# Kernel optimization log

Hardware: AMD Instinct MI355X
Metric: run time of the kernel (lower is better)

The kernel has to match this reference:

```python
import jax, jax.numpy as jnp
import numpy as np

NUM_HEADS = 16
NUM_KV_HEADS = 4
HEAD_DIM = 128
ROPE_DIMS = 64
EPS = 1.1920929e-07  # torch.finfo(float32).eps, used by F.rms_norm(eps=None)


def rms_norm(x):
    ms = jnp.mean(jnp.square(x), axis=-1, keepdims=True)
    return x * jax.lax.rsqrt(ms + EPS)


def apply_rotary(x, cos, sin):
    # x: [..., s, rope_dims]; cos/sin: [s, rope_dims//2]
    h = x.shape[-1] // 2
    x1, x2 = x[..., :h], x[..., h:]
    return jnp.concatenate([x1 * cos + x2 * sin, -x1 * sin + x2 * cos], axis=-1)


def setup_inputs() -> dict:
    key = jax.random.key(0)
    ks = jax.random.split(key, 5)
    b, s, d = 2, 2048, 2048
    return {
        "x": jax.random.normal(ks[0], (b, s, d), jnp.float32),
        "q_w": jax.random.normal(ks[1], (d, d), jnp.float32) * 0.02,
        "k_w": jax.random.normal(ks[2], (NUM_KV_HEADS * HEAD_DIM, d), jnp.float32) * 0.02,
        "v_w": jax.random.normal(ks[3], (NUM_KV_HEADS * HEAD_DIM, d), jnp.float32) * 0.02,
        "out_w": jax.random.normal(ks[4], (d, d), jnp.float32) * 0.02,
        "q_gain": jnp.full((NUM_HEADS,), 12.0, jnp.float32),
    }


def reference(x, q_w, k_w, v_w, out_w, q_gain):
    b, s, d = x.shape
    g = NUM_HEADS // NUM_KV_HEADS

    q = (x @ q_w.T).reshape(b, s, NUM_HEADS, HEAD_DIM).transpose(0, 2, 1, 3)
    k = (x @ k_w.T).reshape(b, s, NUM_KV_HEADS, HEAD_DIM).transpose(0, 2, 1, 3)
    v = (x @ v_w.T).reshape(b, s, NUM_KV_HEADS, HEAD_DIM).transpose(0, 2, 1, 3)

    q = rms_norm(q)
    k = rms_norm(k)

    # partial rotary embedding
    t = jnp.arange(s, dtype=jnp.float32)
    inv_freq = 1.0 / (10000.0 ** (jnp.arange(0, ROPE_DIMS, 2, dtype=jnp.float32) / ROPE_DIMS))
    f = jnp.outer(t, inv_freq)                      # [s, rope_dims//2]
    cos, sin = jnp.cos(f), jnp.sin(f)

    q = jnp.concatenate([apply_rotary(q[..., :ROPE_DIMS], cos, sin), q[..., ROPE_DIMS:]], axis=-1)
    q = q * q_gain[None, :, None, None]
    k = jnp.concatenate([apply_rotary(k[..., :ROPE_DIMS], cos, sin), k[..., ROPE_DIMS:]], axis=-1)

    # GQA-native causal attention (no repeated K/V materialization)
    qg = q.reshape(b, NUM_KV_HEADS, g, s, HEAD_DIM)
    scale = 1.0 / jnp.sqrt(jnp.float32(HEAD_DIM))
    scores = jnp.einsum("bkgqd,bkld->bkgql", qg, k) * scale
    causal = jnp.tril(jnp.ones((s, s), bool))
    scores = jnp.where(causal, scores, jnp.finfo(scores.dtype).min)
    p = jax.nn.softmax(scores, axis=-1)
    y = jnp.einsum("bkgql,bkld->bkgqd", p, v)       # [b, kvh, g, s, hd]
    y = y.reshape(b, NUM_HEADS, s, HEAD_DIM).transpose(0, 2, 1, 3).reshape(b, s, d)
    return y @ out_w.T
```

## Files before the change

### kernel.cpp

```cpp
#include <hip/hip_runtime.h>
#include <cmath>


#define S_LEN 2048
#define DMODEL 2048
#define NH 16
#define NKV 4
#define HD 128

#define NEG_SENT -1.0e30f
#define QK_SCALE 0.08838834764831845f
#define RESCALE_THR 8.0f

typedef _Float16 f16x8 __attribute__((ext_vector_type(8)));
typedef float f32x4 __attribute__((ext_vector_type(4)));

static __device__ __forceinline__ short f2h(float f) {
  _Float16 h = (_Float16)f;
  return *(short*)&h;
}
static __device__ __forceinline__ float h2f(short s) {
  _Float16 h = *(_Float16*)&s;
  return (float)h;
}

static __device__ __forceinline__ void stage16(const short* g, short* ldsbase) {
  __builtin_amdgcn_global_load_lds(
      (const __attribute__((address_space(1))) void*)g,
      (__attribute__((address_space(3))) void*)ldsbase, 16, 0, 0);
}

__global__ __launch_bounds__(256) void f32_to_f16_all(
    const float* __restrict__ s0, const float* __restrict__ s1,
    const float* __restrict__ s2, const float* __restrict__ s3,
    const float* __restrict__ s4, short* __restrict__ d0,
    short* __restrict__ d1, short* __restrict__ d2, short* __restrict__ d3,
    short* __restrict__ d4) {
  int u = blockIdx.x * 256 + threadIdx.x;
  const float* src;
  short* dst;
  int off;
  if (u < 2097152) {
    src = s0; dst = d0; off = u;
  } else if (u < 3145728) {
    src = s1; dst = d1; off = u - 2097152;
  } else if (u < 3407872) {
    src = s2; dst = d2; off = u - 3145728;
  } else if (u < 3670016) {
    src = s3; dst = d3; off = u - 3407872;
  } else {
    src = s4; dst = d4; off = u - 3670016;
  }
  float4 v = *reinterpret_cast<const float4*>(src + (size_t)off * 4);
  short4 o;
  o.x = f2h(v.x); o.y = f2h(v.y); o.z = f2h(v.z); o.w = f2h(v.w);
  *reinterpret_cast<short4*>(dst + (size_t)off * 4) = o;
}

template <bool F32OUT>
static __device__ __forceinline__ void gemm_core(const short* __restrict__ A,
                                                 const short* __restrict__ W,
                                                 void* __restrict__ Cv,
                                                 int N, int K, int bm, int bn) {
  __shared__ __align__(16) short As[2][128][64];
  __shared__ __align__(16) short Ws[2][128][64];
  const int tid = threadIdx.x;
  const int wave = tid >> 6, lane = tid & 63;
  const int quad = lane >> 4, l16 = lane & 15;
  const int wm = (wave >> 1) * 64, wn = (wave & 1) * 64;

  f32x4 acc[4][4];
#pragma unroll
  for (int i = 0; i < 4; i++)
#pragma unroll
    for (int j = 0; j < 4; j++) acc[i][j] = f32x4{0.f, 0.f, 0.f, 0.f};

  const int srow = wave * 8 + (lane >> 3);
  const int scol = (lane & 7) * 8;

  const int NT = K >> 6;

  auto stage_tile = [&](int t, int s) {
    const int k0 = t * 64;
#pragma unroll
    for (int i = 0; i < 4; i++) {
      stage16(A + (size_t)(bm + srow + i * 32) * K + k0 + scol,
              &As[s][wave * 8 + i * 32][0]);
      stage16(W + (size_t)(bn + srow + i * 32) * K + k0 + scol,
              &Ws[s][wave * 8 + i * 32][0]);
    }
  };

  stage_tile(0, 0);

  for (int t = 0; t < NT; t++) {
    const int s = t & 1;
    if (t + 1 < NT) {
      stage_tile(t + 1, s ^ 1);
      asm volatile("s_waitcnt vmcnt(8)" ::: "memory");
    } else {
      asm volatile("s_waitcnt vmcnt(0)" ::: "memory");
    }
    __builtin_amdgcn_s_barrier();

#pragma unroll
    for (int kk = 0; kk < 64; kk += 32) {
      f16x8 af[4], bfr[4];
#pragma unroll
      for (int mi = 0; mi < 4; mi++)
        af[mi] = *reinterpret_cast<const f16x8*>(&As[s][wm + mi * 16 + l16][kk + quad * 8]);
#pragma unroll
      for (int ni = 0; ni < 4; ni++)
        bfr[ni] = *reinterpret_cast<const f16x8*>(&Ws[s][wn + ni * 16 + l16][kk + quad * 8]);
#pragma unroll
      for (int mi = 0; mi < 4; mi++)
#pragma unroll
        for (int ni = 0; ni < 4; ni++)
          acc[mi][ni] = __builtin_amdgcn_mfma_f32_16x16x32_f16(af[mi], bfr[ni], acc[mi][ni], 0, 0, 0);
    }

    if (t + 1 < NT) {
      asm volatile("s_waitcnt lgkmcnt(0)" ::: "memory");
      __builtin_amdgcn_sched_barrier(0);
      __builtin_amdgcn_s_barrier();
    }
  }

#pragma unroll
  for (int mi = 0; mi < 4; mi++)
#pragma unroll
    for (int ni = 0; ni < 4; ni++) {
      int gr = bm + wm + mi * 16 + quad * 4;
      int gc = bn + wn + ni * 16 + l16;
#pragma unroll
      for (int r = 0; r < 4; r++) {
        if (F32OUT)
          ((float*)Cv)[(size_t)(gr + r) * N + gc] = acc[mi][ni][r];
        else
          ((short*)Cv)[(size_t)(gr + r) * N + gc] = f2h(acc[mi][ni][r]);
      }
    }
}

template <bool F32OUT>
__global__ __launch_bounds__(256) void gemm_bt(const short* __restrict__ A,
                                               const short* __restrict__ W,
                                               void* __restrict__ Cv,
                                               int N, int K) {
  gemm_core<F32OUT>(A, W, Cv, N, K, blockIdx.x * 128, blockIdx.y * 128);
}

__global__ __launch_bounds__(256) void gemm_qkv(const short* __restrict__ A,
                                                const short* __restrict__ Wq,
                                                const short* __restrict__ Wk,
                                                const short* __restrict__ Wv,
                                                short* __restrict__ Cq,
                                                short* __restrict__ Ck,
                                                short* __restrict__ Cvp,
                                                int K) {
  const int y = blockIdx.y;
  const short* W;
  short* C;
  int N, bn;
  if (y < 16) {
    W = Wq; C = Cq; N = 2048; bn = y * 128;
  } else if (y < 20) {
    W = Wk; C = Ck; N = 512; bn = (y - 16) * 128;
  } else {
    W = Wv; C = Cvp; N = 512; bn = (y - 20) * 128;
  }
  gemm_core<false>(A, W, (void*)C, N, K, blockIdx.x * 128, bn);
}

__global__ __launch_bounds__(256) void postproc(const short* __restrict__ src,
                                                short* __restrict__ dst,
                                                const float* __restrict__ gain,
                                                int n_heads, int mode) {
  int gw = blockIdx.x * 4 + (threadIdx.x >> 6);
  int lane = threadIdx.x & 63;
  int head = gw % n_heads;
  int token = gw / n_heads;
  int s = token & (S_LEN - 1);
  int b = token >> 11;
  const short* sp = src + (size_t)token * (n_heads * HD) + head * HD;
  float v0 = h2f(sp[lane]);
  float v1 = h2f(sp[lane + 64]);
  float ss = v0 * v0 + v1 * v1;
#pragma unroll
  for (int off = 1; off < 64; off <<= 1) ss += __shfl_xor(ss, off, 64);
  float sc = rsqrtf(ss * (1.0f / 128.0f) + 1.1920929e-07f);
  v0 *= sc;
  v1 *= sc;
  int i = lane & 31;
  float inv = powf(10000.0f, -((float)(2 * i) * (1.0f / 64.0f)));
  float f = (float)s * inv;
  float cs, sn;
  sincosf(f, &sn, &cs);
  float partner = __shfl_xor(v0, 32, 64);
  v0 = (lane < 32) ? (v0 * cs + partner * sn) : (v0 * cs - partner * sn);
  if (mode == 2) {
    float g = gain[head] * QK_SCALE;
    v0 *= g;
    v1 *= g;
  }
  short* dp = dst + ((size_t)(b * n_heads + head) * S_LEN + s) * HD;
  dp[lane] = f2h(v0);
  dp[lane + 64] = f2h(v1);
}

__global__ __launch_bounds__(256) void v_transpose(const short* __restrict__ src,
                                                   short* __restrict__ dst) {
  __shared__ __align__(16) short t[64][72];
  const int tid = threadIdx.x;
  const int s0 = blockIdx.x * 64;
  const int d0 = blockIdx.y * 64;
#pragma unroll
  for (int i = 0; i < 2; i++) {
    int r = (tid >> 3) + i * 32;
    int c = (tid & 7) * 8;
    *reinterpret_cast<int4*>(&t[r][c]) =
        *reinterpret_cast<const int4*>(src + (size_t)(s0 + r) * 512 + d0 + c);
  }
  __syncthreads();
  const int b = s0 >> 11;
  const int sbase = s0 & (S_LEN - 1);
#pragma unroll
  for (int i = 0; i < 2; i++) {
    int dr = (tid >> 3) + i * 32;
    int sc8 = (tid & 7) * 8;
    int d = d0 + dr;
    int kv = d >> 7, dw = d & 127;
    short4 lo, hi;
    lo.x = t[sc8 + 0][dr]; lo.y = t[sc8 + 1][dr];
    lo.z = t[sc8 + 2][dr]; lo.w = t[sc8 + 3][dr];
    hi.x = t[sc8 + 4][dr]; hi.y = t[sc8 + 5][dr];
    hi.z = t[sc8 + 6][dr]; hi.w = t[sc8 + 7][dr];
    short* dp = dst + (((size_t)(b * NKV + kv) * HD + dw) * S_LEN) + sbase + sc8;
    *reinterpret_cast<short4*>(dp) = lo;
    *reinterpret_cast<short4*>(dp + 4) = hi;
  }
}

__global__ __launch_bounds__(256, 2) void attn_fwd(const short* __restrict__ qb,
                                                   const short* __restrict__ kb,
                                                   const short* __restrict__ vT,
                                                   short* __restrict__ out) {
  __shared__ __align__(16) short k_lds[64][136];
  __shared__ __align__(16) short vt_lds[144][72];
  __shared__ __align__(16) short p_lds[4][16][72];

  const int tid = threadIdx.x, wave = tid >> 6, lane = tid & 63;
  const int quad = lane >> 4, l16 = lane & 15;
  const int D = blockIdx.x;
  const int strm = D & 7;
  const int t = D >> 3;
  const int pj = t >> 2;
  const int b = strm >> 2;
  const int kvh = strm & 3;
  const int h = kvh * 4 + (t & 3);

  const short* kptr = kb + ((size_t)(b * NKV + kvh) * S_LEN) * HD;
  const short* vtp  = vT + ((size_t)(b * NKV + kvh) * HD) * S_LEN;

  const int kr = (tid >> 4), kc = (tid & 15) * 8;
  const int vr = (tid >> 3), vc = (tid & 7) * 8;

  {
    int r = 128 + (tid >> 4);
    int c = (tid & 15) * 4;
    short val = (r == 128) ? (short)0x3C00 : (short)0;
    short4 v4 = {val, val, val, val};
    *reinterpret_cast<short4*>(&vt_lds[r][c]) = v4;
  }

  for (int pass = 0; pass < 2; pass++) {
    const int qsub = pass ? (31 - pj) : pj;
    const int q0 = qsub * 64 + wave * 16;
    const short* qptr = qb + ((size_t)(b * NH + h) * S_LEN + q0) * HD;

    f16x8 qf[4];
#pragma unroll
    for (int st = 0; st < 4; st++)
      qf[st] = *reinterpret_cast<const f16x8*>(
          qptr + (size_t)l16 * HD + st * 32 + quad * 8);

    f32x4 o[9];
#pragma unroll
    for (int i = 0; i < 9; i++) o[i] = f32x4{0.f, 0.f, 0.f, 0.f};
    float m_i[4] = {NEG_SENT, NEG_SENT, NEG_SENT, NEG_SENT};

    const int ktiles = qsub + 1;
    for (int kt = 0; kt < ktiles; kt++) {
      const int kbase = kt * 64;
      __syncthreads();
#pragma unroll
      for (int i = 0; i < 4; i++)
        *reinterpret_cast<int4*>(&k_lds[kr + i * 16][kc]) =
            *reinterpret_cast<const int4*>(kptr + (size_t)(kbase + kr + i * 16) * HD + kc);
#pragma unroll
      for (int i = 0; i < 4; i++)
        *reinterpret_cast<int4*>(&vt_lds[vr + i * 32][vc]) =
            *reinterpret_cast<const int4*>(vtp + (size_t)(vr + i * 32) * S_LEN + kbase + vc);
      __syncthreads();

      f32x4 sc[4];
#pragma unroll
      for (int ct = 0; ct < 4; ct++) sc[ct] = f32x4{0.f, 0.f, 0.f, 0.f};
#pragma unroll
      for (int ct = 0; ct < 4; ct++) {
#pragma unroll
        for (int st = 0; st < 4; st++) {
          f16x8 kf = *reinterpret_cast<const f16x8*>(&k_lds[ct * 16 + l16][st * 32 + quad * 8]);
          sc[ct] = __builtin_amdgcn_mfma_f32_16x16x32_f16(qf[st], kf, sc[ct], 0, 0, 0);
        }
      }

      if (kbase + 63 > q0) {
#pragma unroll
        for (int ct = 0; ct < 4; ct++)
#pragma unroll
          for (int r = 0; r < 4; r++) {
            int qrow = q0 + quad * 4 + r;
            int col = kbase + ct * 16 + l16;
            sc[ct][r] = (col <= qrow) ? sc[ct][r] : NEG_SENT;
          }
      }

      float cand[4];
#pragma unroll
      for (int r = 0; r < 4; r++)
        cand[r] = fmaxf(fmaxf(sc[0][r], sc[1][r]), fmaxf(sc[2][r], sc[3][r]));
#pragma unroll
      for (int off = 1; off < 16; off <<= 1)
#pragma unroll
        for (int r = 0; r < 4; r++)
          cand[r] = fmaxf(cand[r], __shfl_xor(cand[r], off, 64));

      bool ch = (cand[0] > m_i[0] + RESCALE_THR) | (cand[1] > m_i[1] + RESCALE_THR) |
                (cand[2] > m_i[2] + RESCALE_THR) | (cand[3] > m_i[3] + RESCALE_THR);
      if (__any(ch)) {
        float alpha[4];
#pragma unroll
        for (int r = 0; r < 4; r++) {
          float mn = fmaxf(m_i[r], cand[r]);
          alpha[r] = __expf(m_i[r] - mn);
          m_i[r] = mn;
        }
#pragma unroll
        for (int nt = 0; nt < 9; nt++)
#pragma unroll
          for (int r = 0; r < 4; r++) o[nt][r] *= alpha[r];
      }

#pragma unroll
      for (int ct = 0; ct < 4; ct++)
#pragma unroll
        for (int r = 0; r < 4; r++) {
          float p = __expf(sc[ct][r] - m_i[r]);
          p_lds[wave][quad * 4 + r][ct * 16 + l16] = f2h(p);
        }

      f16x8 pf0 = *reinterpret_cast<const f16x8*>(&p_lds[wave][l16][quad * 8]);
      f16x8 pf1 = *reinterpret_cast<const f16x8*>(&p_lds[wave][l16][32 + quad * 8]);
#pragma unroll
      for (int nt = 0; nt < 9; nt++) {
        f16x8 vf0 = *reinterpret_cast<const f16x8*>(&vt_lds[nt * 16 + l16][quad * 8]);
        f16x8 vf1 = *reinterpret_cast<const f16x8*>(&vt_lds[nt * 16 + l16][32 + quad * 8]);
        o[nt] = __builtin_amdgcn_mfma_f32_16x16x32_f16(pf0, vf0, o[nt], 0, 0, 0);
        o[nt] = __builtin_amdgcn_mfma_f32_16x16x32_f16(pf1, vf1, o[nt], 0, 0, 0);
      }
    }

    float inv_l[4];
#pragma unroll
    for (int r = 0; r < 4; r++) {
      float l = __shfl(o[8][r], lane & 48, 64);
      inv_l[r] = 1.0f / fmaxf(l, 1e-20f);
    }
#pragma unroll
    for (int nt = 0; nt < 8; nt++)
#pragma unroll
      for (int r = 0; r < 4; r++) {
        int srow = q0 + quad * 4 + r;
        int dcol = nt * 16 + l16;
        out[((size_t)(b * S_LEN + srow)) * DMODEL + h * HD + dcol] =
            f2h(o[nt][r] * inv_l[r]);
      }
  }
}

extern "C" void kernel_launch(void* const* d_in, const int* in_sizes, int n_in,
                              void* d_out, int out_size, void* d_ws, size_t ws_size,
                              hipStream_t stream) {
  const float* x      = (const float*)d_in[0];
  const float* q_w    = (const float*)d_in[1];
  const float* k_w    = (const float*)d_in[2];
  const float* v_w    = (const float*)d_in[3];
  const float* out_w  = (const float*)d_in[4];
  const float* q_gain = (const float*)d_in[5];
  float* out = (float*)d_out;

  const int BS = 2 * S_LEN;
  short* xb   = (short*)d_ws;
  short* wqb  = xb   + (size_t)8 * 1024 * 1024;
  short* wkb  = wqb  + (size_t)4 * 1024 * 1024;
  short* wvb  = wkb  + (size_t)1 * 1024 * 1024;
  short* wob  = wvb  + (size_t)1 * 1024 * 1024;
  short* qraw = wob  + (size_t)4 * 1024 * 1024;
  short* kraw = qraw + (size_t)8 * 1024 * 1024;
  short* vraw = kraw + (size_t)2 * 1024 * 1024;
  short* qbuf = vraw + (size_t)2 * 1024 * 1024;
  short* kbuf = qbuf + (size_t)8 * 1024 * 1024;
  short* vT   = kbuf + (size_t)2 * 1024 * 1024;
  short* attn = qraw;

  dim3 blk(256);
  f32_to_f16_all<<<18432, blk, 0, stream>>>(x, q_w, k_w, v_w, out_w,
                                            xb, wqb, wkb, wvb, wob);

  gemm_qkv<<<dim3(32, 24), blk, 0, stream>>>(xb, wqb, wkb, wvb,
                                             qraw, kraw, vraw, 2048);

  postproc<<<dim3((BS * NH) / 4), blk, 0, stream>>>(qraw, qbuf, q_gain, NH, 2);
  postproc<<<dim3((BS * NKV) / 4), blk, 0, stream>>>(kraw, kbuf, q_gain, NKV, 1);
  v_transpose<<<dim3(BS / 64, 8), blk, 0, stream>>>(vraw, vT);

  attn_fwd<<<dim3(512), blk, 0, stream>>>(qbuf, kbuf, vT, attn);

  gemm_bt<true><<<dim3(32, 16), blk, 0, stream>>>(attn, wob, out, 2048, 2048);
}
```

Measured before the change: 368.3 us.

## Fuse RMSNorm, RoPE, gain and V transpose into QKV GEMM epilogue

The QKV GEMM now stages its 128x128 output tile through shared memory and applies the per-head RMS norm, rotary embedding and gain scaling for Q/K, or writes V transposed, directly from the tile. This removes three separate kernels (two postproc launches and v_transpose) along with the round trip of raw Q/K/V through global memory. The cost is a heavier epilogue with a 64KB shared buffer and a serial per-row loop in each wave, which may reduce occupancy of the GEMM.

```diff
diff --git a/kernel.cpp b/kernel.cpp
--- a/kernel.cpp
+++ b/kernel.cpp
@@ -77,7 +77,6 @@
 
   const int srow = wave * 8 + (lane >> 3);
   const int scol = (lane & 7) * 8;
-
   const int NT = K >> 6;
 
   auto stage_tile = [&](int t, int s) {
@@ -156,88 +155,145 @@
                                                 const short* __restrict__ Wv,
                                                 short* __restrict__ Cq,
                                                 short* __restrict__ Ck,
-                                                short* __restrict__ Cvp,
+                                                short* __restrict__ vT,
+                                                const float* __restrict__ gain,
                                                 int K) {
+  __shared__ __align__(16) char smraw[65536];
+  auto As = reinterpret_cast<short(*)[128][64]>(smraw);
+  auto Ws = reinterpret_cast<short(*)[128][64]>(smraw + 32768);
+  auto ep = reinterpret_cast<short(*)[132]>(smraw);
+
   const int y = blockIdx.y;
   const short* W;
-  short* C;
-  int N, bn;
+  int mode;
+  int bn;
   if (y < 16) {
-    W = Wq; C = Cq; N = 2048; bn = y * 128;
+    W = Wq; bn = y * 128; mode = 2;
   } else if (y < 20) {
-    W = Wk; C = Ck; N = 512; bn = (y - 16) * 128;
+    W = Wk; bn = (y - 16) * 128; mode = 1;
   } else {
-    W = Wv; C = Cvp; N = 512; bn = (y - 20) * 128;
-  }
-  gemm_core<false>(A, W, (void*)C, N, K, blockIdx.x * 128, bn);
-}
-
-__global__ __launch_bounds__(256) void postproc(const short* __restrict__ src,
-                                                short* __restrict__ dst,
-                                                const float* __restrict__ gain,
-                                                int n_heads, int mode) {
-  int gw = blockIdx.x * 4 + (threadIdx.x >> 6);
-  int lane = threadIdx.x & 63;
-  int head = gw % n_heads;
-  int token = gw / n_heads;
-  int s = token & (S_LEN - 1);
-  int b = token >> 11;
-  const short* sp = src + (size_t)token * (n_heads * HD) + head * HD;
-  float v0 = h2f(sp[lane]);
-  float v1 = h2f(sp[lane + 64]);
-  float ss = v0 * v0 + v1 * v1;
-#pragma unroll
-  for (int off = 1; off < 64; off <<= 1) ss += __shfl_xor(ss, off, 64);
-  float sc = rsqrtf(ss * (1.0f / 128.0f) + 1.1920929e-07f);
-  v0 *= sc;
-  v1 *= sc;
-  int i = lane & 31;
-  float inv = powf(10000.0f, -((float)(2 * i) * (1.0f / 64.0f)));
-  float f = (float)s * inv;
-  float cs, sn;
-  sincosf(f, &sn, &cs);
-  float partner = __shfl_xor(v0, 32, 64);
-  v0 = (lane < 32) ? (v0 * cs + partner * sn) : (v0 * cs - partner * sn);
-  if (mode == 2) {
-    float g = gain[head] * QK_SCALE;
-    v0 *= g;
-    v1 *= g;
-  }
-  short* dp = dst + ((size_t)(b * n_heads + head) * S_LEN + s) * HD;
-  dp[lane] = f2h(v0);
-  dp[lane + 64] = f2h(v1);
-}
-
-__global__ __launch_bounds__(256) void v_transpose(const short* __restrict__ src,
-                                                   short* __restrict__ dst) {
-  __shared__ __align__(16) short t[64][72];
+    W = Wv; bn = (y - 20) * 128; mode = 0;
+  }
+  const int bm = blockIdx.x * 128;
+
   const int tid = threadIdx.x;
-  const int s0 = blockIdx.x * 64;
-  const int d0 = blockIdx.y * 64;
-#pragma unroll
-  for (int i = 0; i < 2; i++) {
-    int r = (tid >> 3) + i * 32;
-    int c = (tid & 7) * 8;
-    *reinterpret_cast<int4*>(&t[r][c]) =
-        *reinterpret_cast<const int4*>(src + (size_t)(s0 + r) * 512 + d0 + c);
-  }
+  const int wave = tid >> 6, lane = tid & 63;
+  const int quad = lane >> 4, l16 = lane & 15;
+  const int wm = (wave >> 1) * 64, wn = (wave & 1) * 64;
+
+  f32x4 acc[4][4];
+#pragma unroll
+  for (int i = 0; i < 4; i++)
+#pragma unroll
+    for (int j = 0; j < 4; j++) acc[i][j] = f32x4{0.f, 0.f, 0.f, 0.f};
+
+  const int srow = wave * 8 + (lane >> 3);
+  const int scol = (lane & 7) * 8;
+  const int NT = K >> 6;
+
+  auto stage_tile = [&](int t, int s) {
+    const int k0 = t * 64;
+#pragma unroll
+    for (int i = 0; i < 4; i++) {
+      stage16(A + (size_t)(bm + srow + i * 32) * K + k0 + scol,
+              &As[s][wave * 8 + i * 32][0]);
+      stage16(W + (size_t)(bn + srow + i * 32) * K + k0 + scol,
+              &Ws[s][wave * 8 + i * 32][0]);
+    }
+  };
+
+  stage_tile(0, 0);
+
+  for (int t = 0; t < NT; t++) {
+    const int s = t & 1;
+    if (t + 1 < NT) {
+      stage_tile(t + 1, s ^ 1);
+      asm volatile("s_waitcnt vmcnt(8)" ::: "memory");
+    } else {
+      asm volatile("s_waitcnt vmcnt(0)" ::: "memory");
+    }
+    __builtin_amdgcn_s_barrier();
+
+#pragma unroll
+    for (int kk = 0; kk < 64; kk += 32) {
+      f16x8 af[4], bfr[4];
+#pragma unroll
+      for (int mi = 0; mi < 4; mi++)
+        af[mi] = *reinterpret_cast<const f16x8*>(&As[s][wm + mi * 16 + l16][kk + quad * 8]);
+#pragma unroll
+      for (int ni = 0; ni < 4; ni++)
+        bfr[ni] = *reinterpret_cast<const f16x8*>(&Ws[s][wn + ni * 16 + l16][kk + quad * 8]);
+#pragma unroll
+      for (int mi = 0; mi < 4; mi++)
+#pragma unroll
+        for (int ni = 0; ni < 4; ni++)
+          acc[mi][ni] = __builtin_amdgcn_mfma_f32_16x16x32_f16(af[mi], bfr[ni], acc[mi][ni], 0, 0, 0);
+    }
+
+    if (t + 1 < NT) {
+      asm volatile("s_waitcnt lgkmcnt(0)" ::: "memory");
+      __builtin_amdgcn_sched_barrier(0);
+      __builtin_amdgcn_s_barrier();
+    }
+  }
+
   __syncthreads();
-  const int b = s0 >> 11;
-  const int sbase = s0 & (S_LEN - 1);
-#pragma unroll
-  for (int i = 0; i < 2; i++) {
-    int dr = (tid >> 3) + i * 32;
-    int sc8 = (tid & 7) * 8;
-    int d = d0 + dr;
-    int kv = d >> 7, dw = d & 127;
-    short4 lo, hi;
-    lo.x = t[sc8 + 0][dr]; lo.y = t[sc8 + 1][dr];
-    lo.z = t[sc8 + 2][dr]; lo.w = t[sc8 + 3][dr];
-    hi.x = t[sc8 + 4][dr]; hi.y = t[sc8 + 5][dr];
-    hi.z = t[sc8 + 6][dr]; hi.w = t[sc8 + 7][dr];
-    short* dp = dst + (((size_t)(b * NKV + kv) * HD + dw) * S_LEN) + sbase + sc8;
-    *reinterpret_cast<short4*>(dp) = lo;
-    *reinterpret_cast<short4*>(dp + 4) = hi;
+#pragma unroll
+  for (int mi = 0; mi < 4; mi++)
+#pragma unroll
+    for (int ni = 0; ni < 4; ni++) {
+      const int er = wm + mi * 16 + quad * 4;
+      const int ec = wn + ni * 16 + l16;
+#pragma unroll
+      for (int r = 0; r < 4; r++) ep[er + r][ec] = f2h(acc[mi][ni][r]);
+    }
+  __syncthreads();
+
+  if (mode == 0) {
+    const int d = tid >> 1;
+    const int half = tid & 1;
+    const int kvh2 = y - 20;
+    const int b2 = bm >> 11;
+    const int sbase = bm & (S_LEN - 1);
+    short* dp = vT + (((size_t)(b2 * NKV + kvh2) * HD + d) * S_LEN) + sbase + half * 64;
+#pragma unroll
+    for (int c8 = 0; c8 < 8; c8++) {
+      short vbuf[8];
+#pragma unroll
+      for (int j = 0; j < 8; j++) vbuf[j] = ep[half * 64 + c8 * 8 + j][d];
+      *reinterpret_cast<int4*>(dp + c8 * 8) = *reinterpret_cast<int4*>(vbuf);
+    }
+  } else {
+    const float g = (mode == 2) ? gain[y] * QK_SCALE : 1.0f;
+    short* dstbase = (mode == 2) ? Cq : Ck;
+    const int head = (mode == 2) ? y : (y - 16);
+    const int nh = (mode == 2) ? NH : NKV;
+    const int i2 = lane & 31;
+    const float inv = powf(10000.0f, -((float)(2 * i2) * (1.0f / 64.0f)));
+    for (int j = 0; j < 32; j++) {
+      const int rho = wave * 32 + j;
+      const int token = bm + rho;
+      const int s2 = token & (S_LEN - 1);
+      const int b2 = token >> 11;
+      float v0 = h2f(ep[rho][lane]);
+      float v1 = h2f(ep[rho][lane + 64]);
+      float ss = v0 * v0 + v1 * v1;
+#pragma unroll
+      for (int off = 1; off < 64; off <<= 1) ss += __shfl_xor(ss, off, 64);
+      float scn = rsqrtf(ss * (1.0f / 128.0f) + 1.1920929e-07f);
+      v0 *= scn;
+      v1 *= scn;
+      float f = (float)s2 * inv;
+      float cs, sn;
+      sincosf(f, &sn, &cs);
+      float partner = __shfl_xor(v0, 32, 64);
+      v0 = (lane < 32) ? (v0 * cs + partner * sn) : (v0 * cs - partner * sn);
+      v0 *= g;
+      v1 *= g;
+      short* dp = dstbase + ((size_t)(b2 * nh + head) * S_LEN + s2) * HD;
+      dp[lane] = f2h(v0);
+      dp[lane + 64] = f2h(v1);
+    }
   }
 }
 
@@ -400,30 +456,22 @@
   const float* q_gain = (const float*)d_in[5];
   float* out = (float*)d_out;
 
-  const int BS = 2 * S_LEN;
   short* xb   = (short*)d_ws;
   short* wqb  = xb   + (size_t)8 * 1024 * 1024;
   short* wkb  = wqb  + (size_t)4 * 1024 * 1024;
   short* wvb  = wkb  + (size_t)1 * 1024 * 1024;
   short* wob  = wvb  + (size_t)1 * 1024 * 1024;
-  short* qraw = wob  + (size_t)4 * 1024 * 1024;
-  short* kraw = qraw + (size_t)8 * 1024 * 1024;
-  short* vraw = kraw + (size_t)2 * 1024 * 1024;
-  short* qbuf = vraw + (size_t)2 * 1024 * 1024;
+  short* attn = wob  + (size_t)4 * 1024 * 1024;
+  short* qbuf = attn + (size_t)8 * 1024 * 1024;
   short* kbuf = qbuf + (size_t)8 * 1024 * 1024;
   short* vT   = kbuf + (size_t)2 * 1024 * 1024;
-  short* attn = qraw;
 
   dim3 blk(256);
   f32_to_f16_all<<<18432, blk, 0, stream>>>(x, q_w, k_w, v_w, out_w,
                                             xb, wqb, wkb, wvb, wob);
 
   gemm_qkv<<<dim3(32, 24), blk, 0, stream>>>(xb, wqb, wkb, wvb,
-                                             qraw, kraw, vraw, 2048);
-
-  postproc<<<dim3((BS * NH) / 4), blk, 0, stream>>>(qraw, qbuf, q_gain, NH, 2);
-  postproc<<<dim3((BS * NKV) / 4), blk, 0, stream>>>(kraw, kbuf, q_gain, NKV, 1);
-  v_transpose<<<dim3(BS / 64, 8), blk, 0, stream>>>(vraw, vT);
+                                             qbuf, kbuf, vT, q_gain, 2048);
 
   attn_fwd<<<dim3(512), blk, 0, stream>>>(qbuf, kbuf, vT, attn);
 
```

Result: faster. 348.2 us (-5.5%).
